# Kernel optimization log

Hardware: AMD Instinct MI355X
Metric: run time of the kernel (lower is better)

Reference implementation:

```python
import jax, jax.numpy as jnp
import numpy as np

# convDU3 with stride=1: the torch module loops over height, slicing each row to
# an [n, c, 1, w] tensor and running Conv2d(kernel=(9,1), padding=(4,0)) + ReLU,
# then concatenating rows back along height. Because each per-row input has
# height 1 and is zero-padded to height 9, only the CENTER kernel tap W[:,:,4,0]
# multiplies real data; all other taps multiply zeros. Hence the module is
# mathematically identical to a 1x1 conv with W[:,:,4,0] + bias, then ReLU,
# applied to the full [n, c, h, w] map. We implement that fused form.

CENTER_TAP = 4  # (kernel_h - 1) // 2 for kernel_h = 9


def setup_inputs() -> dict:
    key = jax.random.key(0)
    k1, k2, k3 = jax.random.split(key, 3)
    n, c_in, h, w = 16, 2048, 32, 32
    c_out = 512
    fea = jax.random.normal(k1, (n, c_in, h, w), dtype=jnp.float32)
    # Conv2d weight [out, in, kh, kw] with kaiming-ish scale
    W = jax.random.normal(k2, (c_out, c_in, 9, 1), dtype=jnp.float32) * (1.0 / np.sqrt(c_in * 9))
    b = jax.random.normal(k3, (c_out,), dtype=jnp.float32) * 0.01
    return {"fea": fea, "W": W, "b": b}


def reference(fea, W, b):
    # Only the center tap of the (9,1) kernel contributes (zero padding elsewhere).
    Wc = W[:, :, CENTER_TAP, 0]                      # [c_out, c_in]
    out = jnp.einsum('nchw,oc->nohw', fea, Wc)       # 1x1-conv GEMM
    out = out + b[None, :, None, None]
    return jax.nn.relu(out)
```

## Files before the change

kernel.cpp:

```cpp
#include <hip/hip_runtime.h>

#define C_IN   2048
#define HWSZ   1024
#define NBATCH 16
#define C_OUT  512
#define BM 128
#define BN 128
#define BK 32
#define NKSTEP (C_IN/BK)

typedef __attribute__((ext_vector_type(4))) float f32x4;
typedef __attribute__((ext_vector_type(8))) short bf16x8;

__device__ __forceinline__ unsigned short f2bf(float x){
  unsigned int u = __float_as_uint(x);
  u += 0x7fffu + ((u >> 16) & 1u);
  return (unsigned short)(u >> 16);
}
__device__ __forceinline__ float bf2f(unsigned short h){
  return __uint_as_float(((unsigned int)h) << 16);
}

__global__ void prep_w_kernel(const float* __restrict__ W,
                              unsigned short* __restrict__ Wh,
                              unsigned short* __restrict__ Wl){
  int i = blockIdx.x * 256 + threadIdx.x;
  float x = W[(size_t)i * 9 + 4];
  unsigned short h = f2bf(x);
  Wh[i] = h;
  Wl[i] = f2bf(x - bf2f(h));
}

union FragU { bf16x8 v; uint2 u[2]; };

__global__ __launch_bounds__(256, 2) void gemm_kernel(
    const float* __restrict__ fea,
    const unsigned short* __restrict__ Wh,
    const unsigned short* __restrict__ Wl,
    const float* __restrict__ bias,
    float* __restrict__ out)
{
  __shared__ unsigned short Ah[BM*BK], Al[BM*BK], Bh[BN*BK], Bl[BN*BK];
  __shared__ float bias_s[BM];

  const int t   = threadIdx.x;
  const int l   = t & 63;
  const int wid = t >> 6;
  const int bx  = blockIdx.x;
  const int mt  = bx & 3;
  const int pt  = (bx >> 2) & 7;
  const int nb  = bx >> 5;

  if (t < BM) bias_s[t] = bias[mt*BM + t];

  const unsigned short* whg = Wh + (size_t)mt*BM*C_IN;
  const unsigned short* wlg = Wl + (size_t)mt*BM*C_IN;
  const float* fg = fea + (size_t)nb*C_IN*HWSZ + (size_t)pt*BN;

  const int wr0 = t >> 2;
  const int wh4 = t & 3;
  const int cb  = t >> 5;
  const int pb  = t & 31;

  f32x4 acc[4][4];
  #pragma unroll
  for (int i=0;i<4;i++)
    #pragma unroll
    for (int j=0;j<4;j++) acc[i][j] = (f32x4)0.0f;

  uint4 wvh[2], wvl[2];
  f32x4 fv[4];

  {
    #pragma unroll
    for (int i=0;i<2;i++){
      const size_t ro = (size_t)(wr0 + i*64) * C_IN + wh4*8;
      wvh[i] = *(const uint4*)(whg + ro);
      wvl[i] = *(const uint4*)(wlg + ro);
    }
    #pragma unroll
    for (int i=0;i<4;i++)
      fv[i] = *(const f32x4*)(fg + (size_t)(cb*4 + i)*HWSZ + pb*4);
  }

  const int fr    = l & 15;
  const int o2    = l >> 4;
  const int mrow0 = (wid >> 1) * 64;
  const int ncol0 = (wid & 1) * 64;

  for (int ks = 0; ks < NKSTEP; ks++){
    __syncthreads();
    #pragma unroll
    for (int i=0;i<2;i++){
      const int r    = wr0 + i*64;
      const int key  = (r >> 2) & 7;
      const int base = r * BK;
      uint2 v0, v1;
      v0.x = wvh[i].x; v0.y = wvh[i].y;
      v1.x = wvh[i].z; v1.y = wvh[i].w;
      *(uint2*)&Ah[base + (((wh4*2)    ) ^ key)*4] = v0;
      *(uint2*)&Ah[base + (((wh4*2) + 1) ^ key)*4] = v1;
      v0.x = wvl[i].x; v0.y = wvl[i].y;
      v1.x = wvl[i].z; v1.y = wvl[i].w;
      *(uint2*)&Al[base + (((wh4*2)    ) ^ key)*4] = v0;
      *(uint2*)&Al[base + (((wh4*2) + 1) ^ key)*4] = v1;
    }
    {
      unsigned short hb[4][4], lb[4][4];
      #pragma unroll
      for (int i=0;i<4;i++)
        #pragma unroll
        for (int j=0;j<4;j++){
          float x = fv[i][j];
          unsigned short h = f2bf(x);
          hb[i][j] = h;
          lb[i][j] = f2bf(x - bf2f(h));
        }
      const int g = (cb ^ (pb & 7)) * 4;
      #pragma unroll
      for (int j=0;j<4;j++){
        const int p    = pb*4 + j;
        const int base = p*BK + g;
        uint2 vh, vl;
        vh.x = (unsigned)hb[0][j] | ((unsigned)hb[1][j] << 16);
        vh.y = (unsigned)hb[2][j] | ((unsigned)hb[3][j] << 16);
        vl.x = (unsigned)lb[0][j] | ((unsigned)lb[1][j] << 16);
        vl.y = (unsigned)lb[2][j] | ((unsigned)lb[3][j] << 16);
        *(uint2*)&Bh[base] = vh;
        *(uint2*)&Bl[base] = vl;
      }
    }
    __syncthreads();

    if (ks + 1 < NKSTEP){
      const int c0 = (ks + 1) * BK;
      #pragma unroll
      for (int i=0;i<2;i++){
        const size_t ro = (size_t)(wr0 + i*64) * C_IN + c0 + wh4*8;
        wvh[i] = *(const uint4*)(whg + ro);
        wvl[i] = *(const uint4*)(wlg + ro);
      }
      #pragma unroll
      for (int i=0;i<4;i++)
        fv[i] = *(const f32x4*)(fg + (size_t)(c0 + cb*4 + i)*HWSZ + pb*4);
    }

    FragU ahf[4], alf[4], bhf[4], blf[4];
    #pragma unroll
    for (int mf=0; mf<4; mf++){
      const int r   = mrow0 + mf*16 + fr;
      const int key = (r >> 2) & 7;
      const int b0  = r*BK + ((2*o2    ) ^ key)*4;
      const int b1  = r*BK + ((2*o2 + 1) ^ key)*4;
      ahf[mf].u[0] = *(const uint2*)&Ah[b0];
      ahf[mf].u[1] = *(const uint2*)&Ah[b1];
      alf[mf].u[0] = *(const uint2*)&Al[b0];
      alf[mf].u[1] = *(const uint2*)&Al[b1];
    }
    #pragma unroll
    for (int nf=0; nf<4; nf++){
      const int p   = ncol0 + nf*16 + fr;
      const int key = (p >> 2) & 7;
      const int b0  = p*BK + ((2*o2    ) ^ key)*4;
      const int b1  = p*BK + ((2*o2 + 1) ^ key)*4;
      bhf[nf].u[0] = *(const uint2*)&Bh[b0];
      bhf[nf].u[1] = *(const uint2*)&Bh[b1];
      blf[nf].u[0] = *(const uint2*)&Bl[b0];
      blf[nf].u[1] = *(const uint2*)&Bl[b1];
    }

    #pragma unroll
    for (int mf=0; mf<4; mf++)
      #pragma unroll
      for (int nf=0; nf<4; nf++){
        acc[mf][nf] = __builtin_amdgcn_mfma_f32_16x16x32_bf16(ahf[mf].v, bhf[nf].v, acc[mf][nf], 0, 0, 0);
        acc[mf][nf] = __builtin_amdgcn_mfma_f32_16x16x32_bf16(ahf[mf].v, blf[nf].v, acc[mf][nf], 0, 0, 0);
        acc[mf][nf] = __builtin_amdgcn_mfma_f32_16x16x32_bf16(alf[mf].v, bhf[nf].v, acc[mf][nf], 0, 0, 0);
      }
  }

  float* ob = out + ((size_t)nb*C_OUT + mt*BM) * HWSZ + (size_t)pt*BN;
  #pragma unroll
  for (int mf=0; mf<4; mf++){
    #pragma unroll
    for (int nf=0; nf<4; nf++){
      const int p = ncol0 + nf*16 + fr;
      #pragma unroll
      for (int rr=0; rr<4; rr++){
        const int o = mrow0 + mf*16 + o2*4 + rr;
        float x = acc[mf][nf][rr] + bias_s[o];
        x = fmaxf(x, 0.0f);
        ob[(size_t)o*HWSZ + p] = x;
      }
    }
  }
}

extern "C" void kernel_launch(void* const* d_in, const int* in_sizes, int n_in,
                              void* d_out, int out_size, void* d_ws, size_t ws_size,
                              hipStream_t stream){
  const float* fea = (const float*)d_in[0];
  const float* W   = (const float*)d_in[1];
  const float* b   = (const float*)d_in[2];
  float* out = (float*)d_out;
  unsigned short* Wh = (unsigned short*)d_ws;
  unsigned short* Wl = Wh + (size_t)C_OUT*C_IN;
  prep_w_kernel<<<dim3((C_OUT*C_IN)/256), dim3(256), 0, stream>>>(W, Wh, Wl);
  gemm_kernel<<<dim3(4*8*NBATCH), dim3(256), 0, stream>>>(fea, Wh, Wl, b, out);
}
```

Before: 330.3 us.

## Drop split-bf16 emulation to plain bf16 GEMM, widen BK, remap blocks per XCD

Removes the hi/lo bf16 split for both weights and activations, so each tile needs one MFMA per k-slice instead of three and half the LDS traffic. BK doubles to 64 with 16-byte LDS accesses and a new XOR swizzle. Block indices are remapped so that consecutive blocks on the same XCD share batch and pixel tiles, which is meant to improve L2 reuse. The trade-off is lower precision: plain bf16 inputs with fp32 accumulation may exceed the accuracy tolerance for K=2048.

```diff
diff --git a/kernel.cpp b/kernel.cpp
--- a/kernel.cpp
+++ b/kernel.cpp
@@ -6,7 +6,7 @@
 #define C_OUT  512
 #define BM 128
 #define BN 128
-#define BK 32
+#define BK 64
 #define NKSTEP (C_IN/BK)
 
 typedef __attribute__((ext_vector_type(4))) float f32x4;
@@ -17,44 +17,40 @@
   u += 0x7fffu + ((u >> 16) & 1u);
   return (unsigned short)(u >> 16);
 }
-__device__ __forceinline__ float bf2f(unsigned short h){
-  return __uint_as_float(((unsigned int)h) << 16);
+
+__global__ void prep_w_kernel(const float* __restrict__ W,
+                              unsigned short* __restrict__ Wh){
+  int i = blockIdx.x * 256 + threadIdx.x;
+  Wh[i] = f2bf(W[(size_t)i * 9 + 4]);
 }
 
-__global__ void prep_w_kernel(const float* __restrict__ W,
-                              unsigned short* __restrict__ Wh,
-                              unsigned short* __restrict__ Wl){
-  int i = blockIdx.x * 256 + threadIdx.x;
-  float x = W[(size_t)i * 9 + 4];
-  unsigned short h = f2bf(x);
-  Wh[i] = h;
-  Wl[i] = f2bf(x - bf2f(h));
-}
-
-union FragU { bf16x8 v; uint2 u[2]; };
+union FragU { bf16x8 v; uint4 q; };
 
 __global__ __launch_bounds__(256, 2) void gemm_kernel(
     const float* __restrict__ fea,
     const unsigned short* __restrict__ Wh,
-    const unsigned short* __restrict__ Wl,
     const float* __restrict__ bias,
     float* __restrict__ out)
 {
-  __shared__ unsigned short Ah[BM*BK], Al[BM*BK], Bh[BN*BK], Bl[BN*BK];
+  __shared__ unsigned short Ah[BM*BK];
+  __shared__ unsigned short Bh[BN*BK];
   __shared__ float bias_s[BM];
 
   const int t   = threadIdx.x;
   const int l   = t & 63;
   const int wid = t >> 6;
+
   const int bx  = blockIdx.x;
-  const int mt  = bx & 3;
-  const int pt  = (bx >> 2) & 7;
-  const int nb  = bx >> 5;
+  const int xcd = bx & 7;
+  const int s_  = bx >> 3;
+  const int mt  = s_ & 3;
+  const int pl  = xcd * 16 + (s_ >> 2);
+  const int pt  = pl & 7;
+  const int nb  = pl >> 3;
 
   if (t < BM) bias_s[t] = bias[mt*BM + t];
 
   const unsigned short* whg = Wh + (size_t)mt*BM*C_IN;
-  const unsigned short* wlg = Wl + (size_t)mt*BM*C_IN;
   const float* fg = fea + (size_t)nb*C_IN*HWSZ + (size_t)pt*BN;
 
   const int wr0 = t >> 2;
@@ -68,20 +64,17 @@
     #pragma unroll
     for (int j=0;j<4;j++) acc[i][j] = (f32x4)0.0f;
 
-  uint4 wvh[2], wvl[2];
-  f32x4 fv[4];
+  uint4 wv[2][2];
+  f32x4 fv[8];
 
-  {
+  #pragma unroll
+  for (int i=0;i<2;i++)
     #pragma unroll
-    for (int i=0;i<2;i++){
-      const size_t ro = (size_t)(wr0 + i*64) * C_IN + wh4*8;
-      wvh[i] = *(const uint4*)(whg + ro);
-      wvl[i] = *(const uint4*)(wlg + ro);
-    }
-    #pragma unroll
-    for (int i=0;i<4;i++)
-      fv[i] = *(const f32x4*)(fg + (size_t)(cb*4 + i)*HWSZ + pb*4);
-  }
+    for (int h=0;h<2;h++)
+      wv[i][h] = *(const uint4*)(whg + (size_t)(wr0 + i*64)*C_IN + h*32 + wh4*8);
+  #pragma unroll
+  for (int i=0;i<8;i++)
+    fv[i] = *(const f32x4*)(fg + (size_t)(cb*8 + i)*HWSZ + pb*4);
 
   const int fr    = l & 15;
   const int o2    = l >> 4;
@@ -92,42 +85,30 @@
     __syncthreads();
     #pragma unroll
     for (int i=0;i<2;i++){
-      const int r    = wr0 + i*64;
-      const int key  = (r >> 2) & 7;
-      const int base = r * BK;
-      uint2 v0, v1;
-      v0.x = wvh[i].x; v0.y = wvh[i].y;
-      v1.x = wvh[i].z; v1.y = wvh[i].w;
-      *(uint2*)&Ah[base + (((wh4*2)    ) ^ key)*4] = v0;
-      *(uint2*)&Ah[base + (((wh4*2) + 1) ^ key)*4] = v1;
-      v0.x = wvl[i].x; v0.y = wvl[i].y;
-      v1.x = wvl[i].z; v1.y = wvl[i].w;
-      *(uint2*)&Al[base + (((wh4*2)    ) ^ key)*4] = v0;
-      *(uint2*)&Al[base + (((wh4*2) + 1) ^ key)*4] = v1;
+      const int r   = wr0 + i*64;
+      const int key = (r & 7) << 1;
+      #pragma unroll
+      for (int h=0;h<2;h++){
+        const int q0 = h*8 + wh4*2;
+        *(uint4*)&Ah[r*BK + ((q0 ^ key))*4] = wv[i][h];
+      }
     }
     {
-      unsigned short hb[4][4], lb[4][4];
+      unsigned short hb[8][4];
       #pragma unroll
-      for (int i=0;i<4;i++)
+      for (int i=0;i<8;i++)
         #pragma unroll
-        for (int j=0;j<4;j++){
-          float x = fv[i][j];
-          unsigned short h = f2bf(x);
-          hb[i][j] = h;
-          lb[i][j] = f2bf(x - bf2f(h));
-        }
-      const int g = (cb ^ (pb & 7)) * 4;
+        for (int j=0;j<4;j++) hb[i][j] = f2bf(fv[i][j]);
       #pragma unroll
       for (int j=0;j<4;j++){
-        const int p    = pb*4 + j;
-        const int base = p*BK + g;
-        uint2 vh, vl;
-        vh.x = (unsigned)hb[0][j] | ((unsigned)hb[1][j] << 16);
-        vh.y = (unsigned)hb[2][j] | ((unsigned)hb[3][j] << 16);
-        vl.x = (unsigned)lb[0][j] | ((unsigned)lb[1][j] << 16);
-        vl.y = (unsigned)lb[2][j] | ((unsigned)lb[3][j] << 16);
-        *(uint2*)&Bh[base] = vh;
-        *(uint2*)&Bl[base] = vl;
+        const int p   = pb*4 + j;
+        const int key = (p & 7) << 1;
+        uint4 v;
+        v.x = (unsigned)hb[0][j] | ((unsigned)hb[1][j] << 16);
+        v.y = (unsigned)hb[2][j] | ((unsigned)hb[3][j] << 16);
+        v.z = (unsigned)hb[4][j] | ((unsigned)hb[5][j] << 16);
+        v.w = (unsigned)hb[6][j] | ((unsigned)hb[7][j] << 16);
+        *(uint4*)&Bh[p*BK + (((2*cb) ^ key))*4] = v;
       }
     }
     __syncthreads();
@@ -135,48 +116,40 @@
     if (ks + 1 < NKSTEP){
       const int c0 = (ks + 1) * BK;
       #pragma unroll
-      for (int i=0;i<2;i++){
-        const size_t ro = (size_t)(wr0 + i*64) * C_IN + c0 + wh4*8;
-        wvh[i] = *(const uint4*)(whg + ro);
-        wvl[i] = *(const uint4*)(wlg + ro);
-      }
+      for (int i=0;i<2;i++)
+        #pragma unroll
+        for (int h=0;h<2;h++)
+          wv[i][h] = *(const uint4*)(whg + (size_t)(wr0 + i*64)*C_IN + c0 + h*32 + wh4*8);
       #pragma unroll
-      for (int i=0;i<4;i++)
-        fv[i] = *(const f32x4*)(fg + (size_t)(c0 + cb*4 + i)*HWSZ + pb*4);
+      for (int i=0;i<8;i++)
+        fv[i] = *(const f32x4*)(fg + (size_t)(c0 + cb*8 + i)*HWSZ + pb*4);
     }
 
-    FragU ahf[4], alf[4], bhf[4], blf[4];
+    FragU af[4][2], bff[4][2];
     #pragma unroll
     for (int mf=0; mf<4; mf++){
       const int r   = mrow0 + mf*16 + fr;
-      const int key = (r >> 2) & 7;
-      const int b0  = r*BK + ((2*o2    ) ^ key)*4;
-      const int b1  = r*BK + ((2*o2 + 1) ^ key)*4;
-      ahf[mf].u[0] = *(const uint2*)&Ah[b0];
-      ahf[mf].u[1] = *(const uint2*)&Ah[b1];
-      alf[mf].u[0] = *(const uint2*)&Al[b0];
-      alf[mf].u[1] = *(const uint2*)&Al[b1];
+      const int key = (r & 7) << 1;
+      #pragma unroll
+      for (int s=0; s<2; s++)
+        af[mf][s].q = *(const uint4*)&Ah[r*BK + (((s*8 + 2*o2) ^ key))*4];
     }
     #pragma unroll
     for (int nf=0; nf<4; nf++){
       const int p   = ncol0 + nf*16 + fr;
-      const int key = (p >> 2) & 7;
-      const int b0  = p*BK + ((2*o2    ) ^ key)*4;
-      const int b1  = p*BK + ((2*o2 + 1) ^ key)*4;
-      bhf[nf].u[0] = *(const uint2*)&Bh[b0];
-      bhf[nf].u[1] = *(const uint2*)&Bh[b1];
-      blf[nf].u[0] = *(const uint2*)&Bl[b0];
-      blf[nf].u[1] = *(const uint2*)&Bl[b1];
+      const int key = (p & 7) << 1;
+      #pragma unroll
+      for (int s=0; s<2; s++)
+        bff[nf][s].q = *(const uint4*)&Bh[p*BK + (((s*8 + 2*o2) ^ key))*4];
     }
 
     #pragma unroll
     for (int mf=0; mf<4; mf++)
       #pragma unroll
-      for (int nf=0; nf<4; nf++){
-        acc[mf][nf] = __builtin_amdgcn_mfma_f32_16x16x32_bf16(ahf[mf].v, bhf[nf].v, acc[mf][nf], 0, 0, 0);
-        acc[mf][nf] = __builtin_amdgcn_mfma_f32_16x16x32_bf16(ahf[mf].v, blf[nf].v, acc[mf][nf], 0, 0, 0);
-        acc[mf][nf] = __builtin_amdgcn_mfma_f32_16x16x32_bf16(alf[mf].v, bhf[nf].v, acc[mf][nf], 0, 0, 0);
-      }
+      for (int nf=0; nf<4; nf++)
+        #pragma unroll
+        for (int s=0; s<2; s++)
+          acc[mf][nf] = __builtin_amdgcn_mfma_f32_16x16x32_bf16(af[mf][s].v, bff[nf][s].v, acc[mf][nf], 0, 0, 0);
   }
 
   float* ob = out + ((size_t)nb*C_OUT + mt*BM) * HWSZ + (size_t)pt*BN;
@@ -204,7 +177,6 @@
   const float* b   = (const float*)d_in[2];
   float* out = (float*)d_out;
   unsigned short* Wh = (unsigned short*)d_ws;
-  unsigned short* Wl = Wh + (size_t)C_OUT*C_IN;
-  prep_w_kernel<<<dim3((C_OUT*C_IN)/256), dim3(256), 0, stream>>>(W, Wh, Wl);
-  gemm_kernel<<<dim3(4*8*NBATCH), dim3(256), 0, stream>>>(fea, Wh, Wl, b, out);
+  prep_w_kernel<<<dim3((C_OUT*C_IN)/256), dim3(256), 0, stream>>>(W, Wh);
+  gemm_kernel<<<dim3(4*8*NBATCH), dim3(256), 0, stream>>>(fea, Wh, b, out);
 }
```

New measurement: 306.8 us. 1.08x faster.
